# Performance work log

Measured on AMD Instinct MI355X. Metric: run time of the kernel, lower is better.

Reference implementation:

```python
import jax, jax.numpy as jnp
import numpy as np

N_NODES = 100000
N_EDGES = 3200000
NUM_TYPES = 8
TYPE_DIM = 16
IN_DIM = 5
HID = 64
HEADS = 2
OUT = 64
LN_EPS = 1e-5
NEG_SLOPE = 0.2


def segment_softmax(logits, seg, num_segments):
    # logits: [E, H], seg: [E] destination ids
    m = jax.ops.segment_max(logits, seg, num_segments=num_segments)
    m = jnp.where(jnp.isfinite(m), m, 0.0)
    e = jnp.exp(logits - m[seg])
    s = jax.ops.segment_sum(e, seg, num_segments=num_segments)
    return e / (s[seg] + 1e-16)


def gat_conv(x, W, a_src, a_dst, b, src, dst, n_nodes, heads, ch):
    # x: [N, F_in], W: [F_in, heads*ch], a_src/a_dst: [heads, ch], b: [heads*ch]
    h = (x @ W).reshape(n_nodes, heads, ch)            # [N, H, C]
    al_s = jnp.einsum('nhc,hc->nh', h, a_src)          # [N, H]
    al_d = jnp.einsum('nhc,hc->nh', h, a_dst)          # [N, H]
    e = jax.nn.leaky_relu(al_s[src] + al_d[dst], NEG_SLOPE)  # [E, H]
    alpha = segment_softmax(e, dst, n_nodes)           # [E, H]
    msg = alpha[:, :, None] * h[src]                   # [E, H, C]
    out = jax.ops.segment_sum(msg, dst, num_segments=n_nodes)  # [N, H, C]
    return out.reshape(n_nodes, heads * ch) + b


def setup_inputs() -> dict:
    key = jax.random.key(0)
    ks = jax.random.split(key, 16)
    in1 = IN_DIM + TYPE_DIM  # 21
    inp = {
        'x': jax.random.normal(ks[0], (N_NODES, IN_DIM), dtype=jnp.float32),
        'edge_index': jax.random.randint(ks[1], (2, N_EDGES), 0, N_NODES, dtype=jnp.int32),
        'type_ids': jax.random.randint(ks[2], (N_NODES,), 0, NUM_TYPES, dtype=jnp.int32),
        'type_emb': jax.random.normal(ks[3], (NUM_TYPES, TYPE_DIM), dtype=jnp.float32) * 0.3,
        'W1': jax.random.normal(ks[4], (in1, HID), dtype=jnp.float32) * (1.0 / np.sqrt(in1)),
        'a_src1': jax.random.normal(ks[5], (HEADS, HID // HEADS), dtype=jnp.float32) * 0.1,
        'a_dst1': jax.random.normal(ks[6], (HEADS, HID // HEADS), dtype=jnp.float32) * 0.1,
        'b1': jnp.zeros((HID,), dtype=jnp.float32),
        'W2': jax.random.normal(ks[7], (HID, OUT), dtype=jnp.float32) * (1.0 / np.sqrt(HID)),
        'a_src2': jax.random.normal(ks[8], (1, OUT), dtype=jnp.float32) * 0.1,
        'a_dst2': jax.random.normal(ks[9], (1, OUT), dtype=jnp.float32) * 0.1,
        'b2': jnp.zeros((OUT,), dtype=jnp.float32),
        'gamma': jnp.ones((OUT,), dtype=jnp.float32),
        'beta': jnp.zeros((OUT,), dtype=jnp.float32),
    }
    return inp


def reference(x, type_emb, W1, a_src1, a_dst1, b1, W2, a_src2, a_dst2, b2, gamma, beta, edge_index, type_ids):
    n = x.shape[0]
    # type embedding concat
    xin = jnp.concatenate([x, type_emb[type_ids]], axis=1)  # [N, 21]
    # add self loops (PyG GATConv default)
    loops = jnp.arange(n, dtype=edge_index.dtype)
    src = jnp.concatenate([edge_index[0], loops])
    dst = jnp.concatenate([edge_index[1], loops])
    h = gat_conv(xin, W1, a_src1, a_dst1, b1, src, dst, n, HEADS, HID // HEADS)
    h = jax.nn.relu(h)  # dropout = identity at inference
    h = gat_conv(h, W2, a_src2, a_dst2, b2, src, dst, n, 1, OUT)
    # LayerNorm
    mu = jnp.mean(h, axis=-1, keepdims=True)
    var = jnp.var(h, axis=-1, keepdims=True)
    return (h - mu) / jnp.sqrt(var + LN_EPS) * gamma + beta
```

## Files before the change

kernel.cpp:

```cpp
#include <hip/hip_runtime.h>
#include <hip/hip_fp16.h>

#define NEG_SLOPE 0.2f
#define BKT_SHIFT 8
#define BKT_NODES 256
#define BKT_CAP 10240
#define SRC_SHIFT 18
#define SRC_MASK 0x3FFFF
#define CHUNK 4096
#define NBMAX 512

typedef _Float16 half8 __attribute__((ext_vector_type(8)));
typedef float float4v __attribute__((ext_vector_type(4)));

__global__ void k_node1(const float* __restrict__ x, const int* __restrict__ type_ids,
                        const float* __restrict__ type_emb, const float* __restrict__ W1,
                        const float* __restrict__ a_src1, const float* __restrict__ a_dst1,
                        __half2* __restrict__ h1h, float* __restrict__ als1, float* __restrict__ ald1,
                        int N)
{
    int node = blockIdx.x * 4 + (threadIdx.x >> 6);
    int j = threadIdx.x & 63;
    if (node >= N) return;

    float xin[21];
#pragma unroll
    for (int k = 0; k < 5; k++) xin[k] = x[node * 5 + k];
    int t = type_ids[node];
#pragma unroll
    for (int k = 0; k < 16; k++) xin[5 + k] = type_emb[t * 16 + k];

    float h = 0.f;
#pragma unroll
    for (int k = 0; k < 21; k++) h += xin[k] * W1[k * 64 + j];

    float hn = __shfl_xor(h, 1);
    if ((j & 1) == 0)
        h1h[node * 32 + (j >> 1)] = __floats2half2_rn(h, hn);

    int head = j >> 5, lane = j & 31;
    float ps = h * a_src1[head * 32 + lane];
    float pd = h * a_dst1[head * 32 + lane];
#pragma unroll
    for (int m = 16; m >= 1; m >>= 1) { ps += __shfl_xor(ps, m); pd += __shfl_xor(pd, m); }
    if (lane == 0) { als1[node * 2 + head] = ps; ald1[node * 2 + head] = pd; }
}

__global__ void k_bucketA(const int* __restrict__ ei, unsigned int* __restrict__ pk,
                          int* __restrict__ bcnt, int E, int NBKT)
{
    __shared__ unsigned int stage[CHUNK];
    __shared__ unsigned short stageB[CHUNK];
    __shared__ int cnt[NBMAX];
    __shared__ int excl[NBMAX];
    __shared__ int curp[NBMAX];
    __shared__ int gbase[NBMAX];

    int t = threadIdx.x;
    int e0 = blockIdx.x * CHUNK;
    bool vec4 = ((E & 3) == 0);

    for (int i = t; i < NBMAX; i += 256) cnt[i] = 0;
    __syncthreads();

    int4 s4[4], d4[4];
    bool val[4];

    if (vec4) {
#pragma unroll
        for (int it = 0; it < 4; it++) {
            int e = e0 + it * 1024 + t * 4;
            val[it] = (e < E);
            if (val[it]) {
                s4[it] = *(const int4*)(ei + e);
                d4[it] = *(const int4*)(ei + (size_t)E + e);
                atomicAdd(&cnt[d4[it].x >> BKT_SHIFT], 1);
                atomicAdd(&cnt[d4[it].y >> BKT_SHIFT], 1);
                atomicAdd(&cnt[d4[it].z >> BKT_SHIFT], 1);
                atomicAdd(&cnt[d4[it].w >> BKT_SHIFT], 1);
            }
        }
    } else {
        for (int i = t; i < CHUNK; i += 256) {
            int e = e0 + i;
            if (e >= E) break;
            atomicAdd(&cnt[ei[E + e] >> BKT_SHIFT], 1);
        }
    }
    __syncthreads();
    for (int i = t; i < NBMAX; i += 256) curp[i] = cnt[i];
    __syncthreads();
    for (int off = 1; off < NBMAX; off <<= 1) {
        int v0 = (t >= off) ? cnt[t - off] : 0;
        int v1 = (t + 256 >= off) ? cnt[t + 256 - off] : 0;
        __syncthreads();
        cnt[t] += v0; cnt[t + 256] += v1;
        __syncthreads();
    }
    for (int i = t; i < NBMAX; i += 256) {
        int o = curp[i];
        int ex = cnt[i] - o;
        excl[i] = ex;
        curp[i] = ex;
    }
    __syncthreads();
    for (int b = t; b < NBKT; b += 256) {
        int c = cnt[b] - excl[b];
        gbase[b] = (c > 0) ? atomicAdd(&bcnt[b], c) : 0;
    }
    __syncthreads();
    if (vec4) {
#pragma unroll
        for (int it = 0; it < 4; it++) {
            if (!val[it]) continue;
            int ss[4] = {s4[it].x, s4[it].y, s4[it].z, s4[it].w};
            int dd[4] = {d4[it].x, d4[it].y, d4[it].z, d4[it].w};
#pragma unroll
            for (int k = 0; k < 4; k++) {
                int b = dd[k] >> BKT_SHIFT;
                int p = atomicAdd(&curp[b], 1);
                stage[p] = (unsigned)ss[k] | ((unsigned)(dd[k] & (BKT_NODES - 1)) << SRC_SHIFT);
                stageB[p] = (unsigned short)b;
            }
        }
    } else {
        for (int i = t; i < CHUNK; i += 256) {
            int e = e0 + i;
            if (e >= E) break;
            int s = ei[e], d = ei[E + e];
            int b = d >> BKT_SHIFT;
            int p = atomicAdd(&curp[b], 1);
            stage[p] = (unsigned)s | ((unsigned)(d & (BKT_NODES - 1)) << SRC_SHIFT);
            stageB[p] = (unsigned short)b;
        }
    }
    __syncthreads();
    int total = E - e0; if (total > CHUNK) total = CHUNK;
    for (int i = t; i < total; i += 256) {
        int b = stageB[i];
        int idx = gbase[b] + (i - excl[b]);
        if (idx < BKT_CAP) pk[(size_t)b * BKT_CAP + idx] = stage[i];
    }
}

__global__ void k_build(const unsigned int* __restrict__ pk, const int* __restrict__ bcnt,
                        int* __restrict__ rs, int* __restrict__ cur,
                        int* __restrict__ ssrc, int N)
{
    __shared__ unsigned int vals[BKT_CAP];
    __shared__ int cnt[BKT_NODES];
    __shared__ int cursor[BKT_NODES];
    __shared__ int orig[BKT_NODES];
    __shared__ int red[256];
    int b = blockIdx.x;
    int t = threadIdx.x;
    int nb = min(bcnt[b], BKT_CAP);

    int part = 0;
    for (int i = t; i < b; i += 256) part += min(bcnt[i], BKT_CAP);
    red[t] = part;
    cnt[t] = 0;
    __syncthreads();
    for (int off = 128; off; off >>= 1) {
        if (t < off) red[t] += red[t + off];
        __syncthreads();
    }
    int bs = red[0];

    const unsigned int* mypk = pk + (size_t)b * BKT_CAP;
    int nb4 = nb & ~3;
    for (int e = t * 4; e < nb4; e += 1024) {
        uint4 v = *(const uint4*)(mypk + e);
        *(uint4*)(vals + e) = v;
        atomicAdd(&cnt[v.x >> SRC_SHIFT], 1);
        atomicAdd(&cnt[v.y >> SRC_SHIFT], 1);
        atomicAdd(&cnt[v.z >> SRC_SHIFT], 1);
        atomicAdd(&cnt[v.w >> SRC_SHIFT], 1);
    }
    for (int e = nb4 + t; e < nb; e += 256) {
        unsigned int v = mypk[e];
        vals[e] = v;
        atomicAdd(&cnt[v >> SRC_SHIFT], 1);
    }
    __syncthreads();
    orig[t] = cnt[t];
    __syncthreads();
    for (int off = 1; off < BKT_NODES; off <<= 1) {
        int v = (t >= off) ? cnt[t - off] : 0;
        __syncthreads();
        cnt[t] += v;
        __syncthreads();
    }
    {
        int c = orig[t];
        int ex = cnt[t] - c;
        cursor[t] = ex;
        int node = (b << BKT_SHIFT) + t;
        if (node < N) { rs[node] = bs + ex; cur[node] = bs + ex + c; }
    }
    __syncthreads();
    for (int e = t; e < nb; e += 256) {
        unsigned int w = vals[e];
        int p = atomicAdd(&cursor[w >> SRC_SHIFT], 1);
        ssrc[bs + p] = (int)(w & SRC_MASK);
    }
}

__global__ void k_gather1(const int* __restrict__ rs, const int* __restrict__ cur,
                          const int* __restrict__ ssrc, const float4* __restrict__ h4,
                          const float* __restrict__ als1, const float* __restrict__ ald1,
                          const float* __restrict__ b1, float4* __restrict__ h2h4, int N)
{
    int t = threadIdx.x;
    int wv = t >> 6, l = t & 63;
    int g = l >> 3, i = l & 7;
    int head = i >> 2;
    int grpbase = l & 56;

    int node = blockIdx.x * 32 + wv * 8 + g;
    bool live = node < N;
    int node_c = live ? node : (N - 1);

    int beg = rs[node_c];
    int cnt = live ? (cur[node_c] - beg) : 0;

    float ad0 = ald1[node_c * 2 + 0];
    float ad1 = ald1[node_c * 2 + 1];
    float ad = head ? ad1 : ad0;

    int mc = cnt;
    mc = max(mc, __shfl_xor(mc, 8));
    mc = max(mc, __shfl_xor(mc, 16));
    mc = max(mc, __shfl_xor(mc, 32));

    float acc[8];
#pragma unroll
    for (int k = 0; k < 8; k++) acc[k] = 0.f;
    float wsum = 0.f;

    for (int b = 0; b < mc; b += 8) {
        int slot = b + i;
        bool valid = slot < cnt;
        int idx = valid ? (beg + slot) : 0;
        int s = ssrc[idx];
        if (!valid) s = node_c;
        float2 al = *(const float2*)(als1 + (size_t)s * 2);
        float lg0 = al.x + ad0; lg0 = (lg0 >= 0.f) ? lg0 : NEG_SLOPE * lg0;
        float lg1 = al.y + ad1; lg1 = (lg1 >= 0.f) ? lg1 : NEG_SLOPE * lg1;
        float w0 = valid ? __expf(lg0) : 0.f;
        float w1 = valid ? __expf(lg1) : 0.f;
        __half2 wp = __floats2half2_rn(w0, w1);
        unsigned wpi = *(unsigned*)&wp;

#pragma unroll
        for (int r = 0; r < 8; r++) {
            int sr = __shfl(s, grpbase + r);
            unsigned wri = __shfl(wpi, grpbase + r);
            __half2 wh = *(__half2*)&wri;
            float w = head ? __high2float(wh) : __low2float(wh);
            float4 rv = h4[(size_t)sr * 8 + i];
            const __half* hp = (const __half*)&rv;
#pragma unroll
            for (int k = 0; k < 8; k++)
                acc[k] = fmaf(w, __half2float(hp[k]), acc[k]);
            wsum += w;
        }
    }

    {
        float lg = als1[node_c * 2 + head] + ad;
        lg = (lg >= 0.f) ? lg : NEG_SLOPE * lg;
        float w = __expf(lg);
        float4 rv = h4[(size_t)node_c * 8 + i];
        const __half* hp = (const __half*)&rv;
#pragma unroll
        for (int k = 0; k < 8; k++)
            acc[k] = fmaf(w, __half2float(hp[k]), acc[k]);
        wsum += w;
    }

    float inv = 1.f / (wsum + 1e-16f);
    if (live) {
        union { float4 f4; __half2 h2[4]; } u;
#pragma unroll
        for (int q = 0; q < 4; q++) {
            float v0 = fmaxf(acc[2*q]   * inv + b1[i * 8 + 2*q],     0.f);
            float v1 = fmaxf(acc[2*q+1] * inv + b1[i * 8 + 2*q + 1], 0.f);
            u.h2[q] = __floats2half2_rn(v0, v1);
        }
        h2h4[(size_t)node * 8 + i] = u.f4;
    }
}

__global__ __launch_bounds__(256) void k_node2m(
        const _Float16* __restrict__ h2h, const float* __restrict__ W2,
        const float* __restrict__ a_src2, const float* __restrict__ a_dst2,
        _Float16* __restrict__ h3h, float* __restrict__ als2, float* __restrict__ ald2, int N)
{
    __shared__ _Float16 w2t[64][72];
    __shared__ float h3t[4][16][65];
    int t = threadIdx.x;
    for (int e = t; e < 4096; e += 256) {
        int k = e >> 6, n = e & 63;
        w2t[n][k] = (_Float16)W2[e];
    }
    __syncthreads();

    int w = t >> 6, l = t & 63;
    int l15 = l & 15, quad = l >> 4;
    int nodebase = blockIdx.x * 64 + w * 16;

    int arow = nodebase + l15;
    if (arow >= N) arow = N - 1;
    const half8* ap = (const half8*)(h2h + (size_t)arow * 64 + quad * 8);
    half8 a0 = ap[0];
    half8 a1 = ap[4];
    float4v accs[4];
#pragma unroll
    for (int nt = 0; nt < 4; nt++) {
        half8 b0 = *(const half8*)(&w2t[nt * 16 + l15][quad * 8]);
        half8 b1 = *(const half8*)(&w2t[nt * 16 + l15][32 + quad * 8]);
        float4v c = {0.f, 0.f, 0.f, 0.f};
        c = __builtin_amdgcn_mfma_f32_16x16x32_f16(a0, b0, c, 0, 0, 0);
        c = __builtin_amdgcn_mfma_f32_16x16x32_f16(a1, b1, c, 0, 0, 0);
        accs[nt] = c;
    }
#pragma unroll
    for (int nt = 0; nt < 4; nt++)
#pragma unroll
        for (int r = 0; r < 4; r++)
            h3t[w][quad * 4 + r][nt * 16 + l15] = accs[nt][r];
    __syncthreads();

    int m = l >> 2, part = l & 3;
    int g = blockIdx.x * 64 + w * 16 + m;
    float ps = 0.f, pd = 0.f;
    union { float4 f4[2]; _Float16 h[16]; } u;
#pragma unroll
    for (int c = 0; c < 16; c++) {
        float v = h3t[w][m][part * 16 + c];
        ps += v * a_src2[part * 16 + c];
        pd += v * a_dst2[part * 16 + c];
        u.h[c] = (_Float16)v;
    }
    if (g < N) {
        float4* dst = (float4*)(h3h + (size_t)g * 64) + part * 2;
        dst[0] = u.f4[0];
        dst[1] = u.f4[1];
    }
    ps += __shfl_xor(ps, 1); ps += __shfl_xor(ps, 2);
    pd += __shfl_xor(pd, 1); pd += __shfl_xor(pd, 2);
    if (part == 0 && g < N) { als2[g] = ps; ald2[g] = pd; }
}

__global__ void k_gather2(const int* __restrict__ rs, const int* __restrict__ cur,
                          const int* __restrict__ ssrc, const float4* __restrict__ h4,
                          const float* __restrict__ als2, const float* __restrict__ ald2,
                          const float* __restrict__ b2, const float* __restrict__ gamma,
                          const float* __restrict__ beta, float* __restrict__ out, int N)
{
    int t = threadIdx.x;
    int wv = t >> 6, l = t & 63;
    int g = l >> 3, i = l & 7;
    int grpbase = l & 56;

    int node = blockIdx.x * 32 + wv * 8 + g;
    bool live = node < N;
    int node_c = live ? node : (N - 1);

    int beg = rs[node_c];
    int cnt = live ? (cur[node_c] - beg) : 0;
    float ad = ald2[node_c];

    int mc = cnt;
    mc = max(mc, __shfl_xor(mc, 8));
    mc = max(mc, __shfl_xor(mc, 16));
    mc = max(mc, __shfl_xor(mc, 32));

    float acc[8];
#pragma unroll
    for (int k = 0; k < 8; k++) acc[k] = 0.f;
    float wsum = 0.f;

    for (int b = 0; b < mc; b += 8) {
        int slot = b + i;
        bool valid = slot < cnt;
        int idx = valid ? (beg + slot) : 0;
        int s = ssrc[idx];
        if (!valid) s = node_c;
        float lg = als2[s] + ad;
        lg = (lg >= 0.f) ? lg : NEG_SLOPE * lg;
        float w = valid ? __expf(lg) : 0.f;

#pragma unroll
        for (int r = 0; r < 8; r++) {
            int sr = __shfl(s, grpbase + r);
            float wr = __shfl(w, grpbase + r);
            float4 rv = h4[(size_t)sr * 8 + i];
            const __half* hp = (const __half*)&rv;
#pragma unroll
            for (int k = 0; k < 8; k++)
                acc[k] = fmaf(wr, __half2float(hp[k]), acc[k]);
            wsum += wr;
        }
    }

    {
        float lg = als2[node_c] + ad;
        lg = (lg >= 0.f) ? lg : NEG_SLOPE * lg;
        float w = __expf(lg);
        float4 rv = h4[(size_t)node_c * 8 + i];
        const __half* hp = (const __half*)&rv;
#pragma unroll
        for (int k = 0; k < 8; k++)
            acc[k] = fmaf(w, __half2float(hp[k]), acc[k]);
        wsum += w;
    }

    float inv = 1.f / (wsum + 1e-16f);
    float o[8];
    float s = 0.f;
#pragma unroll
    for (int k = 0; k < 8; k++) { o[k] = acc[k] * inv + b2[i * 8 + k]; s += o[k]; }
    s += __shfl_xor(s, 1); s += __shfl_xor(s, 2); s += __shfl_xor(s, 4);
    float mu = s * (1.f / 64.f);
    float v = 0.f;
#pragma unroll
    for (int k = 0; k < 8; k++) { float d = o[k] - mu; v += d * d; }
    v += __shfl_xor(v, 1); v += __shfl_xor(v, 2); v += __shfl_xor(v, 4);
    v *= (1.f / 64.f);
    float rstd = rsqrtf(v + 1e-5f);
    if (live) {
        float res[8];
#pragma unroll
        for (int k = 0; k < 8; k++)
            res[k] = (o[k] - mu) * rstd * gamma[i * 8 + k] + beta[i * 8 + k];
        float4* op = (float4*)(out + (size_t)node * 64 + i * 8);
        op[0] = make_float4(res[0], res[1], res[2], res[3]);
        op[1] = make_float4(res[4], res[5], res[6], res[7]);
    }
}

extern "C" void kernel_launch(void* const* d_in, const int* in_sizes, int n_in,
                              void* d_out, int out_size, void* d_ws, size_t ws_size,
                              hipStream_t stream) {
    const float* x        = (const float*)d_in[0];
    const int*   ei       = (const int*)  d_in[1];
    const int*   type_ids = (const int*)  d_in[2];
    const float* type_emb = (const float*)d_in[3];
    const float* W1       = (const float*)d_in[4];
    const float* a_src1   = (const float*)d_in[5];
    const float* a_dst1   = (const float*)d_in[6];
    const float* b1       = (const float*)d_in[7];
    const float* W2       = (const float*)d_in[8];
    const float* a_src2   = (const float*)d_in[9];
    const float* a_dst2   = (const float*)d_in[10];
    const float* b2       = (const float*)d_in[11];
    const float* gamma    = (const float*)d_in[12];
    const float* beta     = (const float*)d_in[13];

    int N = in_sizes[0] / 5;
    int E = in_sizes[1] / 2;
    int NBKT = (N + BKT_NODES - 1) >> BKT_SHIFT;

    char* base = (char*)d_ws;
    size_t off = 0;
    auto carve = [&](size_t bytes) { void* p = base + off; off += (bytes + 255) & ~(size_t)255; return p; };
    __half2* h1h = (__half2*)carve((size_t)N * 64 * sizeof(__half));
    size_t pk_bytes = (size_t)NBKT * BKT_CAP * sizeof(unsigned int);
    size_t h23_bytes = 2 * (size_t)N * 64 * sizeof(__half);
    char* uni = (char*)carve(pk_bytes > h23_bytes ? pk_bytes : h23_bytes);
    _Float16* h2h = (_Float16*)uni;
    _Float16* h3h = (_Float16*)(uni + (size_t)N * 64 * sizeof(__half));
    unsigned int* pk = (unsigned int*)uni;
    float* als1  = (float*)carve((size_t)N * 2 * sizeof(float));
    float* ald1  = (float*)carve((size_t)N * 2 * sizeof(float));
    float* als2  = (float*)carve((size_t)N * sizeof(float));
    float* ald2  = (float*)carve((size_t)N * sizeof(float));
    int*   rs    = (int*)carve((size_t)N * sizeof(int));
    int*   cur   = (int*)carve((size_t)N * sizeof(int));
    int*   bcnt  = (int*)carve(1024 * sizeof(int));
    int*   ssrc  = (int*)carve((size_t)E * sizeof(int) + 256);

    dim3 tb(256);

    k_node1<<<dim3((N + 3) / 4), tb, 0, stream>>>(x, type_ids, type_emb, W1, a_src1, a_dst1,
                                                  h1h, als1, ald1, N);

    hipMemsetAsync(bcnt, 0, NBKT * sizeof(int), stream);
    k_bucketA<<<dim3((E + CHUNK - 1) / CHUNK), tb, 0, stream>>>(ei, pk, bcnt, E, NBKT);
    k_build<<<dim3(NBKT), tb, 0, stream>>>(pk, bcnt, rs, cur, ssrc, N);

    dim3 ng((N + 31) / 32);
    k_gather1<<<ng, tb, 0, stream>>>(rs, cur, ssrc, (const float4*)h1h, als1, ald1, b1,
                                     (float4*)h2h, N);
    k_node2m<<<dim3((N + 63) / 64), tb, 0, stream>>>(h2h, W2, a_src2, a_dst2,
                                                     h3h, als2, ald2, N);
    k_gather2<<<ng, tb, 0, stream>>>(rs, cur, ssrc, (const float4*)h3h, als2, ald2, b2,
                                     gamma, beta, (float*)d_out, N);
}
```

Baseline: 324.2 us.

## Use 16 lanes per node in gathers and sort edges by source range

The two gather kernels now give each destination node 16 lanes instead of 8. The two halves each walk a different set of 8 edges and combine their partial sums with a shuffle, which doubles memory-level parallelism per node and halves the number of nodes per block. The bucket build now scatters edges in eight passes, each taking a range of source-id bits, so the CSR source lists come out roughly ordered by source and gather reads get more locality. The cost is eight sweeps over the bucket with extra barriers, plus more wave slots and larger grids for the gathers.

```diff
diff --git a/kernel.cpp b/kernel.cpp
--- a/kernel.cpp
+++ b/kernel.cpp
@@ -199,10 +199,14 @@
         if (node < N) { rs[node] = bs + ex; cur[node] = bs + ex + c; }
     }
     __syncthreads();
-    for (int e = t; e < nb; e += 256) {
-        unsigned int w = vals[e];
-        int p = atomicAdd(&cursor[w >> SRC_SHIFT], 1);
-        ssrc[bs + p] = (int)(w & SRC_MASK);
+    for (int p = 0; p < 8; p++) {
+        for (int e = t; e < nb; e += 256) {
+            unsigned int w = vals[e];
+            if ((int)((w >> 14) & 7u) != p) continue;
+            int q = atomicAdd(&cursor[w >> SRC_SHIFT], 1);
+            ssrc[bs + q] = (int)(w & SRC_MASK);
+        }
+        __syncthreads();
     }
 }
 
@@ -212,12 +216,14 @@
                           const float* __restrict__ b1, float4* __restrict__ h2h4, int N)
 {
     int t = threadIdx.x;
-    int wv = t >> 6, l = t & 63;
-    int g = l >> 3, i = l & 7;
+    int l = t & 63;
+    int q = l & 15;
+    int i = q & 7;
+    int hlf = q >> 3;
+    int grpbase = l & 48;
     int head = i >> 2;
-    int grpbase = l & 56;
-
-    int node = blockIdx.x * 32 + wv * 8 + g;
+
+    int node = blockIdx.x * 16 + (t >> 4);
     bool live = node < N;
     int node_c = live ? node : (N - 1);
 
@@ -229,7 +235,6 @@
     float ad = head ? ad1 : ad0;
 
     int mc = cnt;
-    mc = max(mc, __shfl_xor(mc, 8));
     mc = max(mc, __shfl_xor(mc, 16));
     mc = max(mc, __shfl_xor(mc, 32));
 
@@ -238,8 +243,8 @@
     for (int k = 0; k < 8; k++) acc[k] = 0.f;
     float wsum = 0.f;
 
-    for (int b = 0; b < mc; b += 8) {
-        int slot = b + i;
+    for (int b = 0; b < mc; b += 16) {
+        int slot = b + q;
         bool valid = slot < cnt;
         int idx = valid ? (beg + slot) : 0;
         int s = ssrc[idx];
@@ -254,8 +259,9 @@
 
 #pragma unroll
         for (int r = 0; r < 8; r++) {
-            int sr = __shfl(s, grpbase + r);
-            unsigned wri = __shfl(wpi, grpbase + r);
+            int srcl = grpbase + hlf * 8 + r;
+            int sr = __shfl(s, srcl);
+            unsigned wri = __shfl(wpi, srcl);
             __half2 wh = *(__half2*)&wri;
             float w = head ? __high2float(wh) : __low2float(wh);
             float4 rv = h4[(size_t)sr * 8 + i];
@@ -266,6 +272,10 @@
             wsum += w;
         }
     }
+
+#pragma unroll
+    for (int k = 0; k < 8; k++) acc[k] += __shfl_xor(acc[k], 8);
+    wsum += __shfl_xor(wsum, 8);
 
     {
         float lg = als1[node_c * 2 + head] + ad;
@@ -280,13 +290,13 @@
     }
 
     float inv = 1.f / (wsum + 1e-16f);
-    if (live) {
+    if (live && hlf == 0) {
         union { float4 f4; __half2 h2[4]; } u;
 #pragma unroll
-        for (int q = 0; q < 4; q++) {
-            float v0 = fmaxf(acc[2*q]   * inv + b1[i * 8 + 2*q],     0.f);
-            float v1 = fmaxf(acc[2*q+1] * inv + b1[i * 8 + 2*q + 1], 0.f);
-            u.h2[q] = __floats2half2_rn(v0, v1);
+        for (int c = 0; c < 4; c++) {
+            float v0 = fmaxf(acc[2*c]   * inv + b1[i * 8 + 2*c],     0.f);
+            float v1 = fmaxf(acc[2*c+1] * inv + b1[i * 8 + 2*c + 1], 0.f);
+            u.h2[c] = __floats2half2_rn(v0, v1);
         }
         h2h4[(size_t)node * 8 + i] = u.f4;
     }
@@ -360,11 +370,13 @@
                           const float* __restrict__ beta, float* __restrict__ out, int N)
 {
     int t = threadIdx.x;
-    int wv = t >> 6, l = t & 63;
-    int g = l >> 3, i = l & 7;
-    int grpbase = l & 56;
-
-    int node = blockIdx.x * 32 + wv * 8 + g;
+    int l = t & 63;
+    int q = l & 15;
+    int i = q & 7;
+    int hlf = q >> 3;
+    int grpbase = l & 48;
+
+    int node = blockIdx.x * 16 + (t >> 4);
     bool live = node < N;
     int node_c = live ? node : (N - 1);
 
@@ -373,7 +385,6 @@
     float ad = ald2[node_c];
 
     int mc = cnt;
-    mc = max(mc, __shfl_xor(mc, 8));
     mc = max(mc, __shfl_xor(mc, 16));
     mc = max(mc, __shfl_xor(mc, 32));
 
@@ -382,8 +393,8 @@
     for (int k = 0; k < 8; k++) acc[k] = 0.f;
     float wsum = 0.f;
 
-    for (int b = 0; b < mc; b += 8) {
-        int slot = b + i;
+    for (int b = 0; b < mc; b += 16) {
+        int slot = b + q;
         bool valid = slot < cnt;
         int idx = valid ? (beg + slot) : 0;
         int s = ssrc[idx];
@@ -394,8 +405,9 @@
 
 #pragma unroll
         for (int r = 0; r < 8; r++) {
-            int sr = __shfl(s, grpbase + r);
-            float wr = __shfl(w, grpbase + r);
+            int srcl = grpbase + hlf * 8 + r;
+            int sr = __shfl(s, srcl);
+            float wr = __shfl(w, srcl);
             float4 rv = h4[(size_t)sr * 8 + i];
             const __half* hp = (const __half*)&rv;
 #pragma unroll
@@ -404,6 +416,10 @@
             wsum += wr;
         }
     }
+
+#pragma unroll
+    for (int k = 0; k < 8; k++) acc[k] += __shfl_xor(acc[k], 8);
+    wsum += __shfl_xor(wsum, 8);
 
     {
         float lg = als2[node_c] + ad;
@@ -430,7 +446,7 @@
     v += __shfl_xor(v, 1); v += __shfl_xor(v, 2); v += __shfl_xor(v, 4);
     v *= (1.f / 64.f);
     float rstd = rsqrtf(v + 1e-5f);
-    if (live) {
+    if (live && hlf == 0) {
         float res[8];
 #pragma unroll
         for (int k = 0; k < 8; k++)
@@ -491,7 +507,7 @@
     k_bucketA<<<dim3((E + CHUNK - 1) / CHUNK), tb, 0, stream>>>(ei, pk, bcnt, E, NBKT);
     k_build<<<dim3(NBKT), tb, 0, stream>>>(pk, bcnt, rs, cur, ssrc, N);
 
-    dim3 ng((N + 31) / 32);
+    dim3 ng((N + 15) / 16);
     k_gather1<<<ng, tb, 0, stream>>>(rs, cur, ssrc, (const float4*)h1h, als1, ald1, b1,
                                      (float4*)h2h, N);
     k_node2m<<<dim3((N + 63) / 64), tb, 0, stream>>>(h2h, W2, a_src2, a_dst2,
```

After: 332.4 us. 2.5% more time.
